# Optimization experiments

Hardware: AMD Instinct MI355X
Metric: run time of the kernel (lower is better)

Reference implementation:

```python
import jax, jax.numpy as jnp
import numpy as np


def setup_inputs() -> dict:
    key = jax.random.key(0)
    k1, k2, k3, k4, k5 = jax.random.split(key, 5)
    B, N, C = 16, 1024, 768
    x = jax.random.normal(k1, (B, N, C), dtype=jnp.float32)
    sc_token = jax.random.normal(k2, (1, 196, C), dtype=jnp.float32) * 0.02  # trunc_normal std=0.02
    W_qkv = jax.random.normal(k3, (C, 3 * C), dtype=jnp.float32) * 0.02
    W_proj = jax.random.normal(k4, (C, C), dtype=jnp.float32) * 0.02
    b_proj = jax.random.normal(k5, (C,), dtype=jnp.float32) * 0.02
    return {"x": x, "sc_token": sc_token, "W_qkv": W_qkv, "W_proj": W_proj, "b_proj": b_proj}


def reference(x, sc_token, W_qkv, W_proj, b_proj):
    B, N, C = x.shape
    H = 12
    Dh = C // H
    scale = Dh ** -0.5
    # concat learnable style/content tokens: [B, N1, C]
    xt = jnp.concatenate([x, jnp.broadcast_to(sc_token, (B,) + sc_token.shape[1:])], axis=1)
    N1 = xt.shape[1]
    qkv = (xt @ W_qkv).reshape(B, N1, 3, H, Dh)
    q = qkv[:, :, 0].transpose(0, 2, 1, 3)  # [B,H,N1,Dh]
    k = qkv[:, :, 1].transpose(0, 2, 1, 3)
    v = qkv[:, :, 2].transpose(0, 2, 1, 3)
    attn = jax.nn.softmax(jnp.einsum('bhqd,bhkd->bhqk', q, k) * scale, axis=-1)
    out = jnp.einsum('bhqk,bhkd->bhqd', attn, v)  # [B,H,N1,Dh]
    out = out.transpose(0, 2, 1, 3).reshape(B, N1, C)
    out = out[:, :N, :]  # drop appended tokens
    return out @ W_proj + b_proj
```

## Files before the change

kernel.cpp:

```cpp
#include <hip/hip_runtime.h>
#include <hip/hip_bf16.h>

#define BB 16
#define NN 1024
#define CC 768
#define HH 12
#define DH 64
#define NSC 196
#define N1 1220
#define MPAD 19584
#define M_QKV (BB * N1)
#define N_QKV (3 * CC)
#define M_PROJ (BB * NN)
#define KP 1224

typedef __attribute__((ext_vector_type(8))) short short8;
typedef __attribute__((ext_vector_type(4))) float f32x4;

__device__ __forceinline__ void load_lds16(const void* g, void* l) {
    __builtin_amdgcn_global_load_lds(
        (__attribute__((address_space(1))) void*)(g),
        (__attribute__((address_space(3))) void*)(l),
        16, 0, 0);
}

__global__ __launch_bounds__(256) void cast_xt_kernel(
    const float* __restrict__ x, const float* __restrict__ sct,
    __hip_bfloat16* __restrict__ xt)
{
    const int e   = blockIdx.x * 256 + threadIdx.x;
    const int row = e / 96;
    const int c8  = (e - row * 96) * 8;
    union { short8 s; __hip_bfloat16 h[8]; } u;
    if (row < M_QKV) {
        const int b  = row / N1;
        const int rr = row - b * N1;
        const float* src = (rr < NN)
            ? x   + ((size_t)b * NN + rr) * CC + c8
            : sct + (size_t)(rr - NN) * CC + c8;
        const float4 v0 = *(const float4*)src;
        const float4 v1 = *(const float4*)(src + 4);
        u.h[0] = __float2bfloat16(v0.x); u.h[1] = __float2bfloat16(v0.y);
        u.h[2] = __float2bfloat16(v0.z); u.h[3] = __float2bfloat16(v0.w);
        u.h[4] = __float2bfloat16(v1.x); u.h[5] = __float2bfloat16(v1.y);
        u.h[6] = __float2bfloat16(v1.z); u.h[7] = __float2bfloat16(v1.w);
    } else {
#pragma unroll
        for (int j = 0; j < 8; ++j) u.h[j] = __float2bfloat16(0.f);
    }
    *(short8*)(xt + (size_t)row * CC + c8) = u.s;
}

__global__ __launch_bounds__(256) void cast_wt_kernel(
    const float* __restrict__ W, __hip_bfloat16* __restrict__ WT, int Ncols)
{
    const int e  = blockIdx.x * 256 + threadIdx.x;
    const int n  = e / 96;
    const int k8 = (e - n * 96) * 8;
    union { short8 s; __hip_bfloat16 h[8]; } u;
#pragma unroll
    for (int j = 0; j < 8; ++j)
        u.h[j] = __float2bfloat16(W[(size_t)(k8 + j) * Ncols + n]);
    *(short8*)(WT + (size_t)n * CC + k8) = u.s;
}

__global__ __launch_bounds__(256) void transpose_v_kernel(
    const __hip_bfloat16* __restrict__ qkv, __hip_bfloat16* __restrict__ vt)
{
    __shared__ short Ls[64 * 72];
    const int t  = threadIdx.x;
    const int kt = blockIdx.x, h = blockIdx.y, b = blockIdx.z;
    const __hip_bfloat16* vb = qkv + (size_t)b * N1 * N_QKV + 2 * CC + h * DH;

#pragma unroll
    for (int i = 0; i < 2; ++i) {
        const int c   = t + 256 * i;
        const int key = c >> 3;
        const int d8  = (c & 7) * 8;
        const int kg  = kt * 64 + key;
        union { short8 s; short hh[8]; } u;
        if (kg < N1) {
            u.s = *(const short8*)(vb + (size_t)kg * N_QKV + d8);
        } else {
#pragma unroll
            for (int j = 0; j < 8; ++j) u.hh[j] = 0;
        }
#pragma unroll
        for (int j = 0; j < 8; ++j) Ls[(d8 + j) * 72 + key] = u.hh[j];
    }
    __syncthreads();
    __hip_bfloat16* ob = vt + (size_t)(b * HH + h) * 64 * KP + kt * 64;
#pragma unroll
    for (int i = 0; i < 2; ++i) {
        const int c  = t + 256 * i;
        const int d  = c >> 3;
        const int k8 = (c & 7) * 8;
        if (kt * 64 + k8 < KP)
            *(short8*)(ob + (size_t)d * KP + k8) = *(const short8*)&Ls[d * 72 + k8];
    }
}

template <bool WRITE_BF16>
__global__ __launch_bounds__(256) void mfma_gemm_bt(
    const __hip_bfloat16* __restrict__ A,
    const __hip_bfloat16* __restrict__ BT,
    void* __restrict__ Cout,
    const float* __restrict__ bias,
    int lda, int K, int ldc)
{
    __shared__ __hip_bfloat16 As[128 * 32];
    __shared__ __hip_bfloat16 Bs[128 * 32];

    const int t    = threadIdx.x;
    const int lane = t & 63;
    const int l15  = lane & 15;
    const int quad = lane >> 4;
    const int w    = t >> 6;
    const int wm   = w & 1;
    const int wn   = w >> 1;

    const int n0 = blockIdx.x * 128;
    const int m0 = blockIdx.y * 128;

    const int f0 = t * 16;
    const int r0 = f0 >> 6, c0 = (f0 & 63) >> 1;
    const int r1 = (f0 + 4096) >> 6, c1 = c0;

    const __hip_bfloat16* gA0 = A  + (size_t)(m0 + r0) * lda + c0;
    const __hip_bfloat16* gA1 = A  + (size_t)(m0 + r1) * lda + c1;
    const __hip_bfloat16* gB0 = BT + (size_t)(n0 + r0) * K + c0;
    const __hip_bfloat16* gB1 = BT + (size_t)(n0 + r1) * K + c1;

    __hip_bfloat16* lA0 = As + r0 * 32 + c0;
    __hip_bfloat16* lA1 = As + r1 * 32 + c1;
    __hip_bfloat16* lB0 = Bs + r0 * 32 + c0;
    __hip_bfloat16* lB1 = Bs + r1 * 32 + c1;

    f32x4 acc[4][4];
#pragma unroll
    for (int mi = 0; mi < 4; ++mi)
#pragma unroll
        for (int ni = 0; ni < 4; ++ni) {
            acc[mi][ni][0] = 0.f; acc[mi][ni][1] = 0.f;
            acc[mi][ni][2] = 0.f; acc[mi][ni][3] = 0.f;
        }

    for (int k0 = 0; k0 < K; k0 += 32) {
        __syncthreads();
        load_lds16(gA0, lA0);
        load_lds16(gA1, lA1);
        load_lds16(gB0, lB0);
        load_lds16(gB1, lB1);
        gA0 += 32; gA1 += 32; gB0 += 32; gB1 += 32;
        __syncthreads();

        short8 af[4], bf_[4];
#pragma unroll
        for (int mi = 0; mi < 4; ++mi)
            af[mi] = *(const short8*)&As[(wm * 64 + mi * 16 + l15) * 32 + quad * 8];
#pragma unroll
        for (int ni = 0; ni < 4; ++ni)
            bf_[ni] = *(const short8*)&Bs[(wn * 64 + ni * 16 + l15) * 32 + quad * 8];
#pragma unroll
        for (int mi = 0; mi < 4; ++mi)
#pragma unroll
            for (int ni = 0; ni < 4; ++ni)
                acc[mi][ni] = __builtin_amdgcn_mfma_f32_16x16x32_bf16(
                    af[mi], bf_[ni], acc[mi][ni], 0, 0, 0);
    }

#pragma unroll
    for (int mi = 0; mi < 4; ++mi) {
        const int rowb = m0 + wm * 64 + mi * 16 + quad * 4;
#pragma unroll
        for (int ni = 0; ni < 4; ++ni) {
            const int col = n0 + wn * 64 + ni * 16 + l15;
#pragma unroll
            for (int r = 0; r < 4; ++r) {
                const size_t idx = (size_t)(rowb + r) * ldc + col;
                if (WRITE_BF16)
                    ((__hip_bfloat16*)Cout)[idx] = __float2bfloat16(acc[mi][ni][r]);
                else
                    ((float*)Cout)[idx] = acc[mi][ni][r] + bias[col];
            }
        }
    }
}

__global__ __launch_bounds__(256, 4) void attn_mfma_kernel(
    const __hip_bfloat16* qkv,
    const __hip_bfloat16* __restrict__ vt,
    __hip_bfloat16* ao)
{
    __shared__ __hip_bfloat16 Ks[64 * 64];
    __shared__ __hip_bfloat16 Vs[64 * 64];
    __shared__ short Pl[4 * 16 * 64];

    const int t    = threadIdx.x;
    const int l15  = t & 15;
    const int quad = (t >> 4) & 3;
    const int w    = t >> 6;
    const int swz  = l15 & 7;

    const int qt = blockIdx.x;
    const int h  = blockIdx.y;
    const int b  = blockIdx.z;

    const size_t rowbase = (size_t)b * N1;
    const __hip_bfloat16* qb  = qkv + rowbase * N_QKV + h * DH;
    const __hip_bfloat16* kb  = qkv + rowbase * N_QKV + CC + h * DH;
    const __hip_bfloat16* vtb = vt + (size_t)(b * HH + h) * 64 * KP;

    const int cA = t,       rA = cA >> 3, uA = (cA & 7) ^ (rA & 7);
    const int cB = t + 256, rB = cB >> 3, uB = (cB & 7) ^ (rB & 7);

    short8 qf[2];
    {
        const size_t qrow = (size_t)(qt * 64 + w * 16 + l15);
#pragma unroll
        for (int ks = 0; ks < 2; ++ks)
            qf[ks] = *(const short8*)(qb + qrow * N_QKV + ks * 32 + quad * 8);
    }

    f32x4 oac[4];
#pragma unroll
    for (int dt = 0; dt < 4; ++dt) {
        oac[dt][0] = 0.f; oac[dt][1] = 0.f; oac[dt][2] = 0.f; oac[dt][3] = 0.f;
    }
    float mrun = -1e30f, lrun = 0.f;
    short* Pw = Pl + (w * 16) * 64;

    const float SC2 = 0.18033688011f;

    for (int k0 = 0; k0 < N1; k0 += 64) {
        __syncthreads();
        load_lds16(kb  + (size_t)(k0 + rA) * N_QKV + uA * 8, (char*)Ks + cA * 16);
        load_lds16(kb  + (size_t)(k0 + rB) * N_QKV + uB * 8, (char*)Ks + cB * 16);
        load_lds16(vtb + (size_t)rA * KP + k0 + uA * 8,      (char*)Vs + cA * 16);
        load_lds16(vtb + (size_t)rB * KP + k0 + uB * 8,      (char*)Vs + cB * 16);
        __syncthreads();

        short8 kf[4][2];
#pragma unroll
        for (int mt = 0; mt < 4; ++mt)
#pragma unroll
            for (int ks = 0; ks < 2; ++ks)
                kf[mt][ks] = *(const short8*)
                    &Ks[(mt * 16 + l15) * 64 + ((4 * ks + quad) ^ swz) * 8];

        f32x4 st[4];
#pragma unroll
        for (int mt = 0; mt < 4; ++mt) {
            st[mt][0] = 0.f; st[mt][1] = 0.f; st[mt][2] = 0.f; st[mt][3] = 0.f;
        }
        __builtin_amdgcn_s_setprio(1);
#pragma unroll
        for (int ks = 0; ks < 2; ++ks)
#pragma unroll
            for (int mt = 0; mt < 4; ++mt)
                st[mt] = __builtin_amdgcn_mfma_f32_16x16x32_bf16(
                    kf[mt][ks], qf[ks], st[mt], 0, 0, 0);
        __builtin_amdgcn_s_setprio(0);

        const bool edge = (k0 + 64 > N1);
        float smax = -1e30f;
#pragma unroll
        for (int mt = 0; mt < 4; ++mt)
#pragma unroll
            for (int r = 0; r < 4; ++r) {
                float v = st[mt][r] * SC2;
                if (edge && (k0 + mt * 16 + quad * 4 + r >= N1)) v = -1e30f;
                st[mt][r] = v;
                smax = fmaxf(smax, v);
            }
        smax = fmaxf(smax, __shfl_xor(smax, 16));
        smax = fmaxf(smax, __shfl_xor(smax, 32));
        const float mnew  = fmaxf(mrun, smax);
        const float alpha = exp2f(mrun - mnew);
        float rsum = 0.f;
#pragma unroll
        for (int mt = 0; mt < 4; ++mt)
#pragma unroll
            for (int r = 0; r < 4; ++r) {
                float p = exp2f(st[mt][r] - mnew);
                st[mt][r] = p;
                rsum += p;
            }
        rsum += __shfl_xor(rsum, 16);
        rsum += __shfl_xor(rsum, 32);
        lrun = lrun * alpha + rsum;
        mrun = mnew;

#pragma unroll
        for (int r = 0; r < 4; ++r) {
            const float ar = __shfl(alpha, quad * 4 + r);
#pragma unroll
            for (int dt = 0; dt < 4; ++dt) oac[dt][r] *= ar;
        }

#pragma unroll
        for (int mt = 0; mt < 4; ++mt) {
            union { unsigned long long u; __hip_bfloat16 hh[4]; } pk;
#pragma unroll
            for (int r = 0; r < 4; ++r) pk.hh[r] = __float2bfloat16(st[mt][r]);
            const int unit = (2 * mt + (quad >> 1)) ^ swz;
            *(unsigned long long*)&Pw[l15 * 64 + unit * 8 + (quad & 1) * 4] = pk.u;
        }

        __builtin_amdgcn_s_setprio(1);
#pragma unroll
        for (int ks = 0; ks < 2; ++ks) {
            const short8 pf = *(const short8*)
                &Pw[l15 * 64 + ((4 * ks + quad) ^ swz) * 8];
#pragma unroll
            for (int dt = 0; dt < 4; ++dt) {
                const short8 vf = *(const short8*)
                    &Vs[(l15 + 16 * dt) * 64 + ((4 * ks + quad) ^ swz) * 8];
                oac[dt] = __builtin_amdgcn_mfma_f32_16x16x32_bf16(pf, vf, oac[dt], 0, 0, 0);
            }
        }
        __builtin_amdgcn_s_setprio(0);
    }

    const float li = 1.0f / lrun;
#pragma unroll
    for (int r = 0; r < 4; ++r) {
        const float ir = __shfl(li, quad * 4 + r);
        const int qrow = qt * 64 + w * 16 + quad * 4 + r;
        __hip_bfloat16* orow = ao + ((size_t)b * NN + qrow) * N_QKV + h * DH;
#pragma unroll
        for (int dt = 0; dt < 4; ++dt)
            orow[l15 + 16 * dt] = __float2bfloat16(oac[dt][r] * ir);
    }
}

extern "C" void kernel_launch(void* const* d_in, const int* in_sizes, int n_in,
                              void* d_out, int out_size, void* d_ws, size_t ws_size,
                              hipStream_t stream) {
    const float* x      = (const float*)d_in[0];
    const float* sct    = (const float*)d_in[1];
    const float* W_qkv  = (const float*)d_in[2];
    const float* W_proj = (const float*)d_in[3];
    const float* b_proj = (const float*)d_in[4];
    float* out = (float*)d_out;

    char* p = (char*)d_ws;
    __hip_bfloat16* xt      = (__hip_bfloat16*)p;
    __hip_bfloat16* vtg     = (__hip_bfloat16*)p;
    __hip_bfloat16* qkv     = (__hip_bfloat16*)(p + (size_t)MPAD * CC * 2);
    __hip_bfloat16* WTqkv   = (__hip_bfloat16*)(p + (size_t)MPAD * CC * 2 + (size_t)MPAD * N_QKV * 2);
    __hip_bfloat16* WTproj  = WTqkv + (size_t)N_QKV * CC;
    __hip_bfloat16* ao      = qkv + 2 * CC;

    cast_xt_kernel<<<MPAD * 96 / 256, 256, 0, stream>>>(x, sct, xt);
    cast_wt_kernel<<<N_QKV * 96 / 256, 256, 0, stream>>>(W_qkv, WTqkv, N_QKV);
    cast_wt_kernel<<<CC * 96 / 256, 256, 0, stream>>>(W_proj, WTproj, CC);

    mfma_gemm_bt<true><<<dim3(N_QKV / 128, MPAD / 128), 256, 0, stream>>>(
        xt, WTqkv, qkv, nullptr, CC, CC, N_QKV);
    transpose_v_kernel<<<dim3((N1 + 63) / 64, HH, BB), 256, 0, stream>>>(qkv, vtg);
    attn_mfma_kernel<<<dim3(NN / 64, HH, BB), 256, 0, stream>>>(qkv, vtg, ao);
    mfma_gemm_bt<false><<<dim3(CC / 128, M_PROJ / 128), 256, 0, stream>>>(
        ao, WTproj, out, b_proj, N_QKV, CC, CC);
}
```

Baseline: 416.2 us.

## Use 256x256 triple-buffered GEMM, fold softmax scale into Q, lazy rescale

Both GEMMs move from a 128x128 tile with a single LDS buffer to a 256x256 tile with 512 threads, three LDS stages and prefetching two tiles ahead, plus an XOR swizzle to avoid bank conflicts. This reduces barrier stalls and raises data reuse per tile. The QKV GEMM epilogue now multiplies Q by the softmax scale, which removes a multiply per score in attention. The attention kernel also skips the online-softmax rescale of the output accumulator unless the running max grows by more than 8. The larger tiles give fewer blocks (about 9x77 and 3x64) and use more LDS and registers, which may hurt occupancy and wave balance.

```diff
diff --git a/kernel.cpp b/kernel.cpp
--- a/kernel.cpp
+++ b/kernel.cpp
@@ -8,14 +8,16 @@
 #define DH 64
 #define NSC 196
 #define N1 1220
-#define MPAD 19584
+#define MPAD 19712
 #define M_QKV (BB * N1)
 #define N_QKV (3 * CC)
 #define M_PROJ (BB * NN)
-#define KP 1224
+#define KP 1232
 
 typedef __attribute__((ext_vector_type(8))) short short8;
 typedef __attribute__((ext_vector_type(4))) float f32x4;
+
+#define SC2F 0.18033688011f
 
 __device__ __forceinline__ void load_lds16(const void* g, void* l) {
     __builtin_amdgcn_global_load_lds(
@@ -95,93 +97,119 @@
         const int c  = t + 256 * i;
         const int d  = c >> 3;
         const int k8 = (c & 7) * 8;
-        if (kt * 64 + k8 < KP)
+        if (kt * 64 + k8 + 8 <= KP)
             *(short8*)(ob + (size_t)d * KP + k8) = *(const short8*)&Ls[d * 72 + k8];
     }
 }
 
-template <bool WRITE_BF16>
-__global__ __launch_bounds__(256) void mfma_gemm_bt(
+template <bool WRITE_BF16, bool QSCALE>
+__global__ __launch_bounds__(512, 1) void gemm256(
     const __hip_bfloat16* __restrict__ A,
     const __hip_bfloat16* __restrict__ BT,
     void* __restrict__ Cout,
     const float* __restrict__ bias,
-    int lda, int K, int ldc)
-{
-    __shared__ __hip_bfloat16 As[128 * 32];
-    __shared__ __hip_bfloat16 Bs[128 * 32];
+    int lda, int K, int ldc, int Mvalid)
+{
+    __shared__ __hip_bfloat16 As[3][256 * 32];
+    __shared__ __hip_bfloat16 Bs[3][256 * 32];
 
     const int t    = threadIdx.x;
-    const int lane = t & 63;
-    const int l15  = lane & 15;
-    const int quad = lane >> 4;
+    const int l15  = t & 15;
+    const int quad = (t >> 4) & 3;
     const int w    = t >> 6;
-    const int wm   = w & 1;
-    const int wn   = w >> 1;
-
-    const int n0 = blockIdx.x * 128;
-    const int m0 = blockIdx.y * 128;
-
-    const int f0 = t * 16;
-    const int r0 = f0 >> 6, c0 = (f0 & 63) >> 1;
-    const int r1 = (f0 + 4096) >> 6, c1 = c0;
-
-    const __hip_bfloat16* gA0 = A  + (size_t)(m0 + r0) * lda + c0;
-    const __hip_bfloat16* gA1 = A  + (size_t)(m0 + r1) * lda + c1;
-    const __hip_bfloat16* gB0 = BT + (size_t)(n0 + r0) * K + c0;
-    const __hip_bfloat16* gB1 = BT + (size_t)(n0 + r1) * K + c1;
-
-    __hip_bfloat16* lA0 = As + r0 * 32 + c0;
-    __hip_bfloat16* lA1 = As + r1 * 32 + c1;
-    __hip_bfloat16* lB0 = Bs + r0 * 32 + c0;
-    __hip_bfloat16* lB1 = Bs + r1 * 32 + c1;
-
-    f32x4 acc[4][4];
-#pragma unroll
-    for (int mi = 0; mi < 4; ++mi)
+    const int wm   = w >> 2;
+    const int wn   = w & 3;
+
+    const int n0 = blockIdx.x * 256;
+    const int m0 = blockIdx.y * 256;
+
+    const int r0 = t >> 2;
+    const int su = ((t & 3) ^ (r0 & 3)) * 8;
+    const int lo0 = t * 16;
+
+    const __hip_bfloat16* gA0 = A  + (size_t)(m0 + r0)       * lda + su;
+    const __hip_bfloat16* gA1 = A  + (size_t)(m0 + r0 + 128) * lda + su;
+    const __hip_bfloat16* gB0 = BT + (size_t)(n0 + r0)       * K   + su;
+    const __hip_bfloat16* gB1 = BT + (size_t)(n0 + r0 + 128) * K   + su;
+
+#define STAGE(bi, k0) do {                                          \
+        load_lds16(gA0 + (k0), (char*)&As[(bi)][0] + lo0);          \
+        load_lds16(gA1 + (k0), (char*)&As[(bi)][0] + lo0 + 8192);   \
+        load_lds16(gB0 + (k0), (char*)&Bs[(bi)][0] + lo0);          \
+        load_lds16(gB1 + (k0), (char*)&Bs[(bi)][0] + lo0 + 8192);   \
+    } while (0)
+
+    f32x4 acc[8][4];
+#pragma unroll
+    for (int mi = 0; mi < 8; ++mi)
 #pragma unroll
         for (int ni = 0; ni < 4; ++ni) {
             acc[mi][ni][0] = 0.f; acc[mi][ni][1] = 0.f;
             acc[mi][ni][2] = 0.f; acc[mi][ni][3] = 0.f;
         }
 
-    for (int k0 = 0; k0 < K; k0 += 32) {
-        __syncthreads();
-        load_lds16(gA0, lA0);
-        load_lds16(gA1, lA1);
-        load_lds16(gB0, lB0);
-        load_lds16(gB1, lB1);
-        gA0 += 32; gA1 += 32; gB0 += 32; gB1 += 32;
-        __syncthreads();
-
-        short8 af[4], bf_[4];
-#pragma unroll
-        for (int mi = 0; mi < 4; ++mi)
-            af[mi] = *(const short8*)&As[(wm * 64 + mi * 16 + l15) * 32 + quad * 8];
-#pragma unroll
-        for (int ni = 0; ni < 4; ++ni)
-            bf_[ni] = *(const short8*)&Bs[(wn * 64 + ni * 16 + l15) * 32 + quad * 8];
-#pragma unroll
-        for (int mi = 0; mi < 4; ++mi)
+    STAGE(0, 0);
+    STAGE(1, 32);
+    asm volatile("s_waitcnt vmcnt(4)" ::: "memory");
+    __builtin_amdgcn_s_barrier();
+    __builtin_amdgcn_sched_barrier(0);
+
+    const int NT = K >> 5;
+    int bcur = 0, bpre = 2;
+    for (int tt = 0; tt < NT; ++tt) {
+        if (tt + 2 < NT) STAGE(bpre, (tt + 2) * 32);
+
+        const __hip_bfloat16* Ab = &As[bcur][0];
+        const __hip_bfloat16* Bb = &Bs[bcur][0];
+        short8 af[8], bfr[4];
+#pragma unroll
+        for (int mi = 0; mi < 8; ++mi) {
+            const int row = wm * 128 + mi * 16 + l15;
+            af[mi] = *(const short8*)&Ab[row * 32 + ((quad ^ (row & 3)) << 3)];
+        }
+#pragma unroll
+        for (int ni = 0; ni < 4; ++ni) {
+            const int col = wn * 64 + ni * 16 + l15;
+            bfr[ni] = *(const short8*)&Bb[col * 32 + ((quad ^ (col & 3)) << 3)];
+        }
+
+        __builtin_amdgcn_s_setprio(1);
+#pragma unroll
+        for (int mi = 0; mi < 8; ++mi)
 #pragma unroll
             for (int ni = 0; ni < 4; ++ni)
                 acc[mi][ni] = __builtin_amdgcn_mfma_f32_16x16x32_bf16(
-                    af[mi], bf_[ni], acc[mi][ni], 0, 0, 0);
-    }
-
-#pragma unroll
-    for (int mi = 0; mi < 4; ++mi) {
-        const int rowb = m0 + wm * 64 + mi * 16 + quad * 4;
+                    af[mi], bfr[ni], acc[mi][ni], 0, 0, 0);
+        __builtin_amdgcn_s_setprio(0);
+
+        if (tt + 2 < NT) asm volatile("s_waitcnt vmcnt(4)" ::: "memory");
+        else             asm volatile("s_waitcnt vmcnt(0)" ::: "memory");
+        __builtin_amdgcn_s_barrier();
+        __builtin_amdgcn_sched_barrier(0);
+
+        bcur = (bcur == 2) ? 0 : bcur + 1;
+        bpre = (bpre == 2) ? 0 : bpre + 1;
+    }
+#undef STAGE
+
+#pragma unroll
+    for (int mi = 0; mi < 8; ++mi) {
+        const int rowb = m0 + wm * 128 + mi * 16 + quad * 4;
 #pragma unroll
         for (int ni = 0; ni < 4; ++ni) {
             const int col = n0 + wn * 64 + ni * 16 + l15;
 #pragma unroll
             for (int r = 0; r < 4; ++r) {
-                const size_t idx = (size_t)(rowb + r) * ldc + col;
-                if (WRITE_BF16)
-                    ((__hip_bfloat16*)Cout)[idx] = __float2bfloat16(acc[mi][ni][r]);
-                else
-                    ((float*)Cout)[idx] = acc[mi][ni][r] + bias[col];
+                const int row = rowb + r;
+                if (row < Mvalid) {
+                    float v = acc[mi][ni][r];
+                    if (WRITE_BF16) {
+                        if (QSCALE && n0 < CC) v *= SC2F;
+                        ((__hip_bfloat16*)Cout)[(size_t)row * ldc + col] = __float2bfloat16(v);
+                    } else {
+                        ((float*)Cout)[(size_t)row * ldc + col] = v + bias[col];
+                    }
+                }
             }
         }
     }
@@ -229,8 +257,6 @@
     }
     float mrun = -1e30f, lrun = 0.f;
     short* Pw = Pl + (w * 16) * 64;
-
-    const float SC2 = 0.18033688011f;
 
     for (int k0 = 0; k0 < N1; k0 += 64) {
         __syncthreads();
@@ -268,35 +294,39 @@
         for (int mt = 0; mt < 4; ++mt)
 #pragma unroll
             for (int r = 0; r < 4; ++r) {
-                float v = st[mt][r] * SC2;
+                float v = st[mt][r];
                 if (edge && (k0 + mt * 16 + quad * 4 + r >= N1)) v = -1e30f;
                 st[mt][r] = v;
                 smax = fmaxf(smax, v);
             }
         smax = fmaxf(smax, __shfl_xor(smax, 16));
         smax = fmaxf(smax, __shfl_xor(smax, 32));
-        const float mnew  = fmaxf(mrun, smax);
-        const float alpha = exp2f(mrun - mnew);
+
+        if (!__all(smax - mrun <= 8.0f)) {
+            const float mnew  = fmaxf(mrun, smax);
+            const float alpha = exp2f(mrun - mnew);
+            lrun *= alpha;
+#pragma unroll
+            for (int r = 0; r < 4; ++r) {
+                const float ar = __shfl(alpha, quad * 4 + r);
+#pragma unroll
+                for (int dt = 0; dt < 4; ++dt) oac[dt][r] *= ar;
+            }
+            mrun = mnew;
+        }
+
         float rsum = 0.f;
 #pragma unroll
         for (int mt = 0; mt < 4; ++mt)
 #pragma unroll
             for (int r = 0; r < 4; ++r) {
-                float p = exp2f(st[mt][r] - mnew);
+                float p = exp2f(st[mt][r] - mrun);
                 st[mt][r] = p;
                 rsum += p;
             }
         rsum += __shfl_xor(rsum, 16);
         rsum += __shfl_xor(rsum, 32);
-        lrun = lrun * alpha + rsum;
-        mrun = mnew;
-
-#pragma unroll
-        for (int r = 0; r < 4; ++r) {
-            const float ar = __shfl(alpha, quad * 4 + r);
-#pragma unroll
-            for (int dt = 0; dt < 4; ++dt) oac[dt][r] *= ar;
-        }
+        lrun += rsum;
 
 #pragma unroll
         for (int mt = 0; mt < 4; ++mt) {
@@ -348,7 +378,7 @@
     __hip_bfloat16* xt      = (__hip_bfloat16*)p;
     __hip_bfloat16* vtg     = (__hip_bfloat16*)p;
     __hip_bfloat16* qkv     = (__hip_bfloat16*)(p + (size_t)MPAD * CC * 2);
-    __hip_bfloat16* WTqkv   = (__hip_bfloat16*)(p + (size_t)MPAD * CC * 2 + (size_t)MPAD * N_QKV * 2);
+    __hip_bfloat16* WTqkv   = (__hip_bfloat16*)(p + (size_t)MPAD * CC * 2 + (size_t)M_QKV * N_QKV * 2);
     __hip_bfloat16* WTproj  = WTqkv + (size_t)N_QKV * CC;
     __hip_bfloat16* ao      = qkv + 2 * CC;
 
@@ -356,10 +386,10 @@
     cast_wt_kernel<<<N_QKV * 96 / 256, 256, 0, stream>>>(W_qkv, WTqkv, N_QKV);
     cast_wt_kernel<<<CC * 96 / 256, 256, 0, stream>>>(W_proj, WTproj, CC);
 
-    mfma_gemm_bt<true><<<dim3(N_QKV / 128, MPAD / 128), 256, 0, stream>>>(
-        xt, WTqkv, qkv, nullptr, CC, CC, N_QKV);
+    gemm256<true, true><<<dim3(N_QKV / 256, MPAD / 256), 512, 0, stream>>>(
+        xt, WTqkv, qkv, nullptr, CC, CC, N_QKV, M_QKV);
     transpose_v_kernel<<<dim3((N1 + 63) / 64, HH, BB), 256, 0, stream>>>(qkv, vtg);
     attn_mfma_kernel<<<dim3(NN / 64, HH, BB), 256, 0, stream>>>(qkv, vtg, ao);
-    mfma_gemm_bt<false><<<dim3(CC / 128, M_PROJ / 128), 256, 0, stream>>>(
-        ao, WTproj, out, b_proj, N_QKV, CC, CC);
-}
+    gemm256<false, false><<<dim3(CC / 256, M_PROJ / 256), 512, 0, stream>>>(
+        ao, WTproj, out, b_proj, N_QKV, CC, CC, M_PROJ);
+}
```

Measured after the change: 432.4 us. +3.9%, slower.
